# Kernel tuning notes

Measured on AMD Instinct MI355X. Metric: run time of the kernel, lower is better.

Reference implementation:

```python
import jax, jax.numpy as jnp
import numpy as np

N_EMBEDS = 1024
N_HEADS = 16
HEAD_DIM = N_EMBEDS // N_HEADS
SCALE = HEAD_DIM ** (-0.5)
B, T = 2, 2048


def setup_inputs() -> dict:
    key = jax.random.key(0)
    k1, k2, k3, k4 = jax.random.split(key, 4)
    x = jax.random.normal(k1, (B, T, N_EMBEDS), dtype=jnp.float32)
    # Glorot-uniform-style init like keras Dense defaults (scale irrelevant for correctness)
    w_qkv = jax.random.normal(k2, (N_EMBEDS, 3 * N_EMBEDS), dtype=jnp.float32) * (N_EMBEDS ** -0.5)
    w_proj = jax.random.normal(k3, (N_EMBEDS, N_EMBEDS), dtype=jnp.float32) * (N_EMBEDS ** -0.5)
    b_proj = jnp.zeros((N_EMBEDS,), dtype=jnp.float32)
    return {"x": x, "w_qkv": w_qkv, "w_proj": w_proj, "b_proj": b_proj}


def reference(x, w_qkv, w_proj, b_proj):
    Bc, Tc, D = x.shape
    qkv = x @ w_qkv                                   # [B,T,3D]
    q, k, v = jnp.split(qkv, 3, axis=-1)
    def heads(t):
        return t.reshape(Bc, Tc, N_HEADS, HEAD_DIM).transpose(0, 2, 1, 3)  # [B,H,T,hd]
    q, k, v = heads(q), heads(k), heads(v)
    att = jnp.einsum("bhqd,bhkd->bhqk", q, k) * SCALE  # [B,H,T,T]
    causal = jnp.tril(jnp.ones((Tc, Tc), dtype=bool))[None, None]
    att = jnp.where(causal, att, jnp.float32(-1e9))
    att = jax.nn.softmax(att, axis=-1)
    out = jnp.einsum("bhqk,bhkd->bhqd", att, v)        # [B,H,T,hd]
    out = out.transpose(0, 2, 1, 3).reshape(Bc, Tc, D)
    return out @ w_proj + b_proj
```

## Files before the change

### kernel.cpp

```cpp
#include <hip/hip_runtime.h>
#include <hip/hip_bf16.h>


typedef __bf16 bf16;
typedef float f32x4 __attribute__((ext_vector_type(4)));
typedef float f32x16 __attribute__((ext_vector_type(16)));
typedef bf16 bf16x4 __attribute__((ext_vector_type(4)));
typedef bf16 bf16x8 __attribute__((ext_vector_type(8)));

#define B_ 2
#define T_ 2048
#define D_ 1024
#define H_ 16
#define HD_ 64
#define QSPLIT 9

__device__ __forceinline__ f32x16 mfma32(bf16x8 a, bf16x8 b, f32x16 c) {
    return __builtin_amdgcn_mfma_f32_32x32x16_bf16(a, b, c, 0, 0, 0);
}

__device__ __forceinline__ void gload16(void* l, const void* g) {
    __builtin_amdgcn_global_load_lds(
        (const __attribute__((address_space(1))) unsigned int*)g,
        (__attribute__((address_space(3))) unsigned int*)l, 16, 0, 0);
}

__device__ __forceinline__ f32x16 z16() {
    f32x16 v;
#pragma unroll
    for (int i = 0; i < 16; ++i) v[i] = 0.f;
    return v;
}

__global__ __launch_bounds__(256) void cast_f32_bf16(const float* __restrict__ in,
                                                     bf16* __restrict__ out, int n4) {
    int i = blockIdx.x * 256 + threadIdx.x;
    if (i < n4) {
        float4 v = ((const float4*)in)[i];
        bf16x4 o = { (bf16)v.x, (bf16)v.y, (bf16)v.z, (bf16)v.w };
        ((bf16x4*)out)[i] = o;
    }
}

__global__ __launch_bounds__(256) void cast_transpose(const float* __restrict__ in,
                                                      bf16* __restrict__ out, int R, int C) {
    __shared__ float tile[32][33];
    int cx = blockIdx.x * 32 + threadIdx.x;
    int r0 = blockIdx.y * 32;
#pragma unroll
    for (int j = 0; j < 32; j += 8)
        tile[threadIdx.y + j][threadIdx.x] = in[(size_t)(r0 + threadIdx.y + j) * C + cx];
    __syncthreads();
    int rx = r0 + threadIdx.x;
    int c0 = blockIdx.x * 32;
#pragma unroll
    for (int j = 0; j < 32; j += 8)
        out[(size_t)(c0 + threadIdx.y + j) * R + rx] = (bf16)tile[threadIdx.x][threadIdx.y + j];
}

__global__ __launch_bounds__(256) void transpose_v(const bf16* __restrict__ vb,
                                                   bf16* __restrict__ vt) {
    __shared__ bf16 st[64 * 65];
    const int bh = blockIdx.y;
    const int t0 = blockIdx.x * 64;
    const int tid = threadIdx.x;
#pragma unroll
    for (int c = 0; c < 2; ++c) {
        int cid = tid + c * 256;
        int r = cid >> 3, col = (cid & 7) * 8;
        bf16x8 v = *(const bf16x8*)&vb[((size_t)bh * T_ + t0 + r) * HD_ + col];
#pragma unroll
        for (int j = 0; j < 8; ++j) st[r * 65 + col + j] = v[j];
    }
    __syncthreads();
#pragma unroll
    for (int c = 0; c < 2; ++c) {
        int cid = tid + c * 256;
        int tg = cid & 7, d = cid >> 3;
        bf16x8 o;
#pragma unroll
        for (int j = 0; j < 8; ++j) o[j] = st[(tg * 8 + j) * 65 + d];
        *(bf16x8*)&vt[((size_t)bh * HD_ + d) * T_ + t0 + tg * 8] = o;
    }
}

template <int MW, int NWN, int EPI>
__global__ __launch_bounds__(256) void gemm_k(
    const bf16* __restrict__ A, const bf16* __restrict__ Bt,
    int M, int N, int K,
    bf16* __restrict__ qb, bf16* __restrict__ kb, bf16* __restrict__ vb,
    const float* __restrict__ bias, float* __restrict__ outf) {
    constexpr int BM = 64 * MW;
    constexpr int BN = 64 * NWN;
    __shared__ bf16 sA[BM * 64];
    __shared__ bf16 sB[BN * 64];
    const int tid = threadIdx.x;
    const int wave = tid >> 6, lane = tid & 63;
    const int ln = lane & 31, hi = lane >> 5;
    const int wr = (wave >> 1) * (32 * MW);
    const int wc = (wave & 1) * (32 * NWN);
    const int m0 = blockIdx.x * BM, n0 = blockIdx.y * BN;

    f32x16 acc[MW][NWN];
#pragma unroll
    for (int mi = 0; mi < MW; ++mi)
#pragma unroll
        for (int ni = 0; ni < NWN; ++ni) acc[mi][ni] = z16();

    for (int k0 = 0; k0 < K; k0 += 64) {
        __syncthreads();
#pragma unroll
        for (int j = 0; j < 2 * MW; ++j) {
            int c = tid + 256 * j;
            int r = c >> 3, g = (c & 7) ^ (r & 7);
            gload16(&sA[c * 8], A + (size_t)(m0 + r) * K + k0 + 8 * g);
        }
#pragma unroll
        for (int j = 0; j < 2 * NWN; ++j) {
            int c = tid + 256 * j;
            int r = c >> 3, g = (c & 7) ^ (r & 7);
            gload16(&sB[c * 8], Bt + (size_t)(n0 + r) * K + k0 + 8 * g);
        }
        __syncthreads();
#pragma unroll
        for (int s = 0; s < 4; ++s) {
            bf16x8 av[MW], bv[NWN];
#pragma unroll
            for (int mi = 0; mi < MW; ++mi) {
                int r = wr + mi * 32 + ln;
                av[mi] = *(const bf16x8*)((const char*)sA + r * 128 +
                                          ((((s << 1) | hi) ^ (r & 7)) << 4));
            }
#pragma unroll
            for (int ni = 0; ni < NWN; ++ni) {
                int r = wc + ni * 32 + ln;
                bv[ni] = *(const bf16x8*)((const char*)sB + r * 128 +
                                          ((((s << 1) | hi) ^ (r & 7)) << 4));
            }
#pragma unroll
            for (int mi = 0; mi < MW; ++mi)
#pragma unroll
                for (int ni = 0; ni < NWN; ++ni)
                    acc[mi][ni] = mfma32(av[mi], bv[ni], acc[mi][ni]);
        }
    }

#pragma unroll
    for (int mi = 0; mi < MW; ++mi)
#pragma unroll
        for (int ni = 0; ni < NWN; ++ni)
#pragma unroll
            for (int r = 0; r < 16; ++r) {
                int row = m0 + wr + mi * 32 + (r & 3) + 8 * (r >> 2) + 4 * hi;
                int col = n0 + wc + ni * 32 + ln;
                float v = acc[mi][ni][r];
                if (EPI == 0) {
                    int part = col >> 10, h = (col >> 6) & 15, d = col & 63;
                    int b = row >> 11, t = row & (T_ - 1);
                    size_t idx = ((size_t)(b * H_ + h) * T_ + t) * HD_ + d;
                    bf16* dst = (part == 0) ? qb : (part == 1) ? kb : vb;
                    dst[idx] = (bf16)v;
                } else {
                    outf[(size_t)row * N + col] = v + bias[col];
                }
            }
}

__device__ __forceinline__ bf16x8 kread(const char* base, int row, int s, int hi) {
    int b = (row * 128 + s * 32 + hi * 16) ^ ((row & 7) << 4);
    return *(const bf16x8*)(base + b);
}
__device__ __forceinline__ bf16x8 vread(const char* base, int row, int s, int hi) {
    int sw = (row & 7) << 4;
    int b0 = (row * 128 + s * 32 + hi * 8) ^ sw;
    int b1 = (row * 128 + s * 32 + hi * 8 + 16) ^ sw;
    bf16x4 lo = *(const bf16x4*)(base + b0);
    bf16x4 hi4 = *(const bf16x4*)(base + b1);
    return __builtin_shufflevector(lo, hi4, 0, 1, 2, 3, 4, 5, 6, 7);
}

__global__ __launch_bounds__(256) void attn_kernel(
    const bf16* __restrict__ qb, const bf16* __restrict__ kb,
    const bf16* __restrict__ vtb, bf16* __restrict__ ob,
    bf16* __restrict__ oP, float2* __restrict__ mlP) {
    __shared__ bf16 sK2[2][4096];
    __shared__ bf16 sV2[2][4096];

    const int bid = blockIdx.x;
    const int bh = bid & 31;
    const int sid = bid >> 5;
    int qt, seg, t0, t1;
    if (sid < QSPLIT) {
        qt = sid; seg = -1; t0 = 0; t1 = 2 * qt + 2;
    } else {
        int idx = sid - QSPLIT;
        qt = QSPLIT + (idx >> 1);
        seg = idx & 1;
        if (seg == 0) { t0 = 0; t1 = qt + 1; }
        else          { t0 = qt + 1; t1 = 2 * qt + 2; }
    }
    const int b = bh >> 4, h = bh & 15;
    const int tid = threadIdx.x, wave = tid >> 6, lane = tid & 63;
    const int ln = lane & 31, hi = lane >> 5;
    const int qs = qt * 128 + wave * 32;
    const int qrow = qs + ln;

    const bf16* Qg = qb + (size_t)bh * (T_ * HD_);
    const bf16* Kg = kb + (size_t)bh * (T_ * HD_);
    const bf16* Vtg = vtb + (size_t)bh * (HD_ * T_);

    bf16x8 qf[4];
#pragma unroll
    for (int s = 0; s < 4; ++s) {
        bf16x8 v = *(const bf16x8*)&Qg[(size_t)qrow * HD_ + s * 16 + hi * 8];
#pragma unroll
        for (int e = 0; e < 8; ++e) v[e] = (bf16)((float)v[e] * 0.1803368801f);
        qf[s] = v;
    }

    const int srow = tid >> 3;
    const int scol = (tid & 7) * 8;
    const int kw0 = (srow * 128 + (tid & 7) * 16) ^ ((srow & 7) << 4);
    const int kw1 = ((srow + 32) * 128 + (tid & 7) * 16) ^ ((srow & 7) << 4);

    {
        int kv0 = t0 * 64;
        bf16x8 k0 = *(const bf16x8*)&Kg[(size_t)(kv0 + srow) * HD_ + scol];
        bf16x8 k1 = *(const bf16x8*)&Kg[(size_t)(kv0 + srow + 32) * HD_ + scol];
        bf16x8 v0 = *(const bf16x8*)&Vtg[(size_t)srow * T_ + kv0 + scol];
        bf16x8 v1 = *(const bf16x8*)&Vtg[(size_t)(srow + 32) * T_ + kv0 + scol];
        *(bf16x8*)((char*)sK2[0] + kw0) = k0;
        *(bf16x8*)((char*)sK2[0] + kw1) = k1;
        *(bf16x8*)((char*)sV2[0] + kw0) = v0;
        *(bf16x8*)((char*)sV2[0] + kw1) = v1;
    }
    __syncthreads();

    const float NINF = -__builtin_inff();
    f32x16 oA = z16(), oB = z16();
    float mR = NINF, lR = 0.f;
    int cur = 0;

    for (int t = t0; t < t1; ++t) {
        bf16x8 kr0, kr1, vr0, vr1;
        const bool pf = (t + 1) < t1;
        if (pf) {
            int kv0 = (t + 1) * 64;
            kr0 = *(const bf16x8*)&Kg[(size_t)(kv0 + srow) * HD_ + scol];
            kr1 = *(const bf16x8*)&Kg[(size_t)(kv0 + srow + 32) * HD_ + scol];
            vr0 = *(const bf16x8*)&Vtg[(size_t)srow * T_ + kv0 + scol];
            vr1 = *(const bf16x8*)&Vtg[(size_t)(srow + 32) * T_ + kv0 + scol];
        }

        if (64 * t <= qs + 31) {
            const char* kbase = (const char*)sK2[cur];
            const char* vbase = (const char*)sV2[cur];

            f32x16 p0 = z16(), p1 = z16();
#pragma unroll
            for (int s = 0; s < 4; ++s) {
                bf16x8 a0 = kread(kbase, ln, s, hi);
                bf16x8 a1 = kread(kbase, ln + 32, s, hi);
                p0 = mfma32(a0, qf[s], p0);
                p1 = mfma32(a1, qf[s], p1);
            }

            if (64 * t + 63 > qs) {
                int kvb = 64 * t + 4 * hi;
#pragma unroll
                for (int r = 0; r < 16; ++r) {
                    int kvr = kvb + (r & 3) + 8 * (r >> 2);
                    if (kvr > qrow) p0[r] = NINF;
                    if (kvr + 32 > qrow) p1[r] = NINF;
                }
            }

            float mx0 = NINF, mx1 = NINF, mx2 = NINF, mx3 = NINF;
#pragma unroll
            for (int r = 0; r < 16; r += 4) {
                mx0 = fmaxf(mx0, p0[r]);     mx1 = fmaxf(mx1, p0[r + 1]);
                mx2 = fmaxf(mx2, p0[r + 2]); mx3 = fmaxf(mx3, p0[r + 3]);
                mx0 = fmaxf(mx0, p1[r]);     mx1 = fmaxf(mx1, p1[r + 1]);
                mx2 = fmaxf(mx2, p1[r + 2]); mx3 = fmaxf(mx3, p1[r + 3]);
            }
            float pm = fmaxf(fmaxf(mx0, mx1), fmaxf(mx2, mx3));
            pm = fmaxf(pm, __shfl_xor(pm, 32));

            if (__any(pm > mR + 8.f)) {
                float mnew = fmaxf(mR, pm);
                float fac = exp2f(mR - mnew);
                lR *= fac;
#pragma unroll
                for (int r = 0; r < 16; ++r) { oA[r] *= fac; oB[r] *= fac; }
                mR = mnew;
            }

            float s0 = 0.f, s1 = 0.f, s2 = 0.f, s3 = 0.f;
#pragma unroll
            for (int r = 0; r < 16; r += 4) {
                p0[r] = exp2f(p0[r] - mR);         s0 += p0[r];
                p0[r + 1] = exp2f(p0[r + 1] - mR); s1 += p0[r + 1];
                p0[r + 2] = exp2f(p0[r + 2] - mR); s2 += p0[r + 2];
                p0[r + 3] = exp2f(p0[r + 3] - mR); s3 += p0[r + 3];
                p1[r] = exp2f(p1[r] - mR);         s0 += p1[r];
                p1[r + 1] = exp2f(p1[r + 1] - mR); s1 += p1[r + 1];
                p1[r + 2] = exp2f(p1[r + 2] - mR); s2 += p1[r + 2];
                p1[r + 3] = exp2f(p1[r + 3] - mR); s3 += p1[r + 3];
            }
            float rs = (s0 + s1) + (s2 + s3);
            rs += __shfl_xor(rs, 32);
            lR += rs;

            bf16x8 pa0, pa1, pa2, pa3;
#pragma unroll
            for (int e = 0; e < 8; ++e) {
                pa0[e] = (bf16)p0[e];
                pa1[e] = (bf16)p0[8 + e];
                pa2[e] = (bf16)p1[e];
                pa3[e] = (bf16)p1[8 + e];
            }

#pragma unroll
            for (int s = 0; s < 4; ++s) {
                bf16x8 pas = (s == 0) ? pa0 : (s == 1) ? pa1 : (s == 2) ? pa2 : pa3;
                oA = mfma32(vread(vbase, ln, s, hi), pas, oA);
                oB = mfma32(vread(vbase, ln + 32, s, hi), pas, oB);
            }
        }

        if (pf) {
            int nb = cur ^ 1;
            *(bf16x8*)((char*)sK2[nb] + kw0) = kr0;
            *(bf16x8*)((char*)sK2[nb] + kw1) = kr1;
            *(bf16x8*)((char*)sV2[nb] + kw0) = vr0;
            *(bf16x8*)((char*)sV2[nb] + kw1) = vr1;
        }
        __syncthreads();
        cur ^= 1;
    }

    if (seg < 0) {
        float inv = 1.f / lR;
        bf16* orow = ob + ((size_t)(b * T_ + qrow)) * D_ + h * HD_;
#pragma unroll
        for (int g = 0; g < 4; ++g) {
            bf16x4 w, w2;
#pragma unroll
            for (int j = 0; j < 4; ++j) {
                w[j] = (bf16)(oA[4 * g + j] * inv);
                w2[j] = (bf16)(oB[4 * g + j] * inv);
            }
            *(bf16x4*)&orow[4 * hi + 8 * g] = w;
            *(bf16x4*)&orow[32 + 4 * hi + 8 * g] = w2;
        }
    } else {
        int row = wave * 32 + ln;
        size_t sbase = (((size_t)bh * (16 - QSPLIT) + (qt - QSPLIT)) * 2 + seg);
        bf16* prow = oP + (sbase * 128 + row) * 64;
#pragma unroll
        for (int g = 0; g < 4; ++g) {
            bf16x4 w, w2;
#pragma unroll
            for (int j = 0; j < 4; ++j) {
                w[j] = (bf16)oA[4 * g + j];
                w2[j] = (bf16)oB[4 * g + j];
            }
            *(bf16x4*)&prow[4 * hi + 8 * g] = w;
            *(bf16x4*)&prow[32 + 4 * hi + 8 * g] = w2;
        }
        if (hi == 0) mlP[sbase * 128 + row] = make_float2(mR, lR);
    }
}

__global__ __launch_bounds__(256) void attn_merge(
    const bf16* __restrict__ oP, const float2* __restrict__ mlP,
    bf16* __restrict__ ob) {
    constexpr int NQS = 16 - QSPLIT;
    int gid = blockIdx.x * 256 + threadIdx.x;
    int bh = gid / (NQS * 128);
    int rem = gid - bh * (NQS * 128);
    int qi = rem >> 7, row = rem & 127;
    int b = bh >> 4, h = bh & 15;
    int t = (QSPLIT + qi) * 128 + row;
    size_t sbase = ((size_t)bh * NQS + qi) * 2;
    float2 ml0 = mlP[(sbase + 0) * 128 + row];
    float2 ml1 = mlP[(sbase + 1) * 128 + row];
    float ms = fmaxf(ml0.x, ml1.x);
    float w0 = exp2f(ml0.x - ms), w1 = exp2f(ml1.x - ms);
    float inv = 1.f / (ml0.y * w0 + ml1.y * w1);
    w0 *= inv; w1 *= inv;
    const bf16* r0 = oP + ((sbase + 0) * 128 + row) * 64;
    const bf16* r1 = oP + ((sbase + 1) * 128 + row) * 64;
    bf16* dst = ob + ((size_t)(b * T_ + t)) * D_ + h * HD_;
#pragma unroll
    for (int g = 0; g < 8; ++g) {
        bf16x8 a = *(const bf16x8*)&r0[g * 8];
        bf16x8 c = *(const bf16x8*)&r1[g * 8];
        bf16x8 o;
#pragma unroll
        for (int j = 0; j < 8; ++j)
            o[j] = (bf16)((float)a[j] * w0 + (float)c[j] * w1);
        *(bf16x8*)&dst[g * 8] = o;
    }
}

extern "C" void kernel_launch(void* const* d_in, const int* in_sizes, int n_in,
                              void* d_out, int out_size, void* d_ws, size_t ws_size,
                              hipStream_t stream) {
    const float* x = (const float*)d_in[0];
    const float* w_qkv = (const float*)d_in[1];
    const float* w_proj = (const float*)d_in[2];
    const float* b_proj = (const float*)d_in[3];
    float* out = (float*)d_out;
    char* ws = (char*)d_ws;

    bf16* xb = (bf16*)(ws);
    bf16* ob = (bf16*)(ws);
    bf16* wqkvt = (bf16*)(ws + 8388608);
    bf16* vtbuf = (bf16*)(ws + 8388608);
    bf16* qbuf = (bf16*)(ws + 16777216);
    bf16* wprojt = (bf16*)(ws + 16777216);
    bf16* kbuf = (bf16*)(ws + 25165824);
    bf16* vbuf = (bf16*)(ws + 33554432);
    bf16* oP = (bf16*)(ws + 33554432);
    float2* mlP = (float2*)(ws + 33554432 + 7340032);

    cast_f32_bf16<<<4096, 256, 0, stream>>>(x, xb, (B_ * T_ * D_) / 4);
    dim3 tb(32, 8);
    cast_transpose<<<dim3(3 * D_ / 32, D_ / 32), tb, 0, stream>>>(w_qkv, wqkvt, D_, 3 * D_);

    gemm_k<2, 2, 0><<<dim3((B_ * T_) / 128, (3 * D_) / 128), 256, 0, stream>>>(
        xb, wqkvt, B_ * T_, 3 * D_, D_, qbuf, kbuf, vbuf, nullptr, nullptr);

    transpose_v<<<dim3(T_ / 64, B_ * H_), 256, 0, stream>>>(vbuf, vtbuf);

    attn_kernel<<<23 * 32, 256, 0, stream>>>(qbuf, kbuf, vtbuf, ob, oP, mlP);
    attn_merge<<<112, 256, 0, stream>>>(oP, mlP, ob);

    cast_transpose<<<dim3(D_ / 32, D_ / 32), tb, 0, stream>>>(w_proj, wprojt, D_, D_);

    gemm_k<1, 2, 1><<<dim3((B_ * T_) / 64, D_ / 128), 256, 0, stream>>>(
        ob, wprojt, B_ * T_, D_, D_, nullptr, nullptr, nullptr, b_proj, out);
}
```

Baseline: 135.7 us.

## Stream K/V tiles into LDS via direct global_load_lds with swizzled source addresses

Replaces the register-staged K/V prefetch (global load to VGPRs, then ds_write after compute) with direct global-to-LDS loads into the alternate buffer. The XOR swizzle moves from the LDS write address to the global source column. It also adds s_setprio around the MFMA blocks, fuses exp2 with the bf16 packing of P, and requests 3 blocks per CU through launch_bounds. The aim is to cut VGPR pressure and LDS-write instructions and raise occupancy, at the cost of register spilling if the cap at 3 waves is too tight.

```diff
diff --git a/kernel.cpp b/kernel.cpp
--- a/kernel.cpp
+++ b/kernel.cpp
@@ -179,7 +179,7 @@
     return __builtin_shufflevector(lo, hi4, 0, 1, 2, 3, 4, 5, 6, 7);
 }
 
-__global__ __launch_bounds__(256) void attn_kernel(
+__global__ __launch_bounds__(256, 3) void attn_kernel(
     const bf16* __restrict__ qb, const bf16* __restrict__ kb,
     const bf16* __restrict__ vtb, bf16* __restrict__ ob,
     bf16* __restrict__ oP, float2* __restrict__ mlP) {
@@ -218,21 +218,15 @@
         qf[s] = v;
     }
 
-    const int srow = tid >> 3;
-    const int scol = (tid & 7) * 8;
-    const int kw0 = (srow * 128 + (tid & 7) * 16) ^ ((srow & 7) << 4);
-    const int kw1 = ((srow + 32) * 128 + (tid & 7) * 16) ^ ((srow & 7) << 4);
+    const int rr0 = tid >> 3;
+    const int gg = ((tid & 7) ^ (rr0 & 7)) * 8;
 
     {
         int kv0 = t0 * 64;
-        bf16x8 k0 = *(const bf16x8*)&Kg[(size_t)(kv0 + srow) * HD_ + scol];
-        bf16x8 k1 = *(const bf16x8*)&Kg[(size_t)(kv0 + srow + 32) * HD_ + scol];
-        bf16x8 v0 = *(const bf16x8*)&Vtg[(size_t)srow * T_ + kv0 + scol];
-        bf16x8 v1 = *(const bf16x8*)&Vtg[(size_t)(srow + 32) * T_ + kv0 + scol];
-        *(bf16x8*)((char*)sK2[0] + kw0) = k0;
-        *(bf16x8*)((char*)sK2[0] + kw1) = k1;
-        *(bf16x8*)((char*)sV2[0] + kw0) = v0;
-        *(bf16x8*)((char*)sV2[0] + kw1) = v1;
+        gload16(&sK2[0][tid * 8], Kg + (size_t)(kv0 + rr0) * HD_ + gg);
+        gload16(&sK2[0][(tid + 256) * 8], Kg + (size_t)(kv0 + rr0 + 32) * HD_ + gg);
+        gload16(&sV2[0][tid * 8], Vtg + (size_t)rr0 * T_ + kv0 + gg);
+        gload16(&sV2[0][(tid + 256) * 8], Vtg + (size_t)(rr0 + 32) * T_ + kv0 + gg);
     }
     __syncthreads();
 
@@ -242,14 +236,14 @@
     int cur = 0;
 
     for (int t = t0; t < t1; ++t) {
-        bf16x8 kr0, kr1, vr0, vr1;
-        const bool pf = (t + 1) < t1;
-        if (pf) {
+        if ((t + 1) < t1) {
             int kv0 = (t + 1) * 64;
-            kr0 = *(const bf16x8*)&Kg[(size_t)(kv0 + srow) * HD_ + scol];
-            kr1 = *(const bf16x8*)&Kg[(size_t)(kv0 + srow + 32) * HD_ + scol];
-            vr0 = *(const bf16x8*)&Vtg[(size_t)srow * T_ + kv0 + scol];
-            vr1 = *(const bf16x8*)&Vtg[(size_t)(srow + 32) * T_ + kv0 + scol];
+            bf16* kd = sK2[cur ^ 1];
+            bf16* vd = sV2[cur ^ 1];
+            gload16(&kd[tid * 8], Kg + (size_t)(kv0 + rr0) * HD_ + gg);
+            gload16(&kd[(tid + 256) * 8], Kg + (size_t)(kv0 + rr0 + 32) * HD_ + gg);
+            gload16(&vd[tid * 8], Vtg + (size_t)rr0 * T_ + kv0 + gg);
+            gload16(&vd[(tid + 256) * 8], Vtg + (size_t)(rr0 + 32) * T_ + kv0 + gg);
         }
 
         if (64 * t <= qs + 31) {
@@ -257,6 +251,7 @@
             const char* vbase = (const char*)sV2[cur];
 
             f32x16 p0 = z16(), p1 = z16();
+            __builtin_amdgcn_s_setprio(1);
 #pragma unroll
             for (int s = 0; s < 4; ++s) {
                 bf16x8 a0 = kread(kbase, ln, s, hi);
@@ -264,6 +259,7 @@
                 p0 = mfma32(a0, qf[s], p0);
                 p1 = mfma32(a1, qf[s], p1);
             }
+            __builtin_amdgcn_s_setprio(0);
 
             if (64 * t + 63 > qs) {
                 int kvb = 64 * t + 4 * hi;
@@ -296,45 +292,28 @@
             }
 
             float s0 = 0.f, s1 = 0.f, s2 = 0.f, s3 = 0.f;
-#pragma unroll
-            for (int r = 0; r < 16; r += 4) {
-                p0[r] = exp2f(p0[r] - mR);         s0 += p0[r];
-                p0[r + 1] = exp2f(p0[r + 1] - mR); s1 += p0[r + 1];
-                p0[r + 2] = exp2f(p0[r + 2] - mR); s2 += p0[r + 2];
-                p0[r + 3] = exp2f(p0[r + 3] - mR); s3 += p0[r + 3];
-                p1[r] = exp2f(p1[r] - mR);         s0 += p1[r];
-                p1[r + 1] = exp2f(p1[r + 1] - mR); s1 += p1[r + 1];
-                p1[r + 2] = exp2f(p1[r + 2] - mR); s2 += p1[r + 2];
-                p1[r + 3] = exp2f(p1[r + 3] - mR); s3 += p1[r + 3];
+            bf16x8 pa0, pa1, pa2, pa3;
+#pragma unroll
+            for (int e = 0; e < 8; ++e) {
+                float a = exp2f(p0[e] - mR);      s0 += a;  pa0[e] = (bf16)a;
+                float bb = exp2f(p0[8 + e] - mR); s1 += bb; pa1[e] = (bf16)bb;
+                float c = exp2f(p1[e] - mR);      s2 += c;  pa2[e] = (bf16)c;
+                float d = exp2f(p1[8 + e] - mR);  s3 += d;  pa3[e] = (bf16)d;
             }
             float rs = (s0 + s1) + (s2 + s3);
             rs += __shfl_xor(rs, 32);
             lR += rs;
 
-            bf16x8 pa0, pa1, pa2, pa3;
-#pragma unroll
-            for (int e = 0; e < 8; ++e) {
-                pa0[e] = (bf16)p0[e];
-                pa1[e] = (bf16)p0[8 + e];
-                pa2[e] = (bf16)p1[e];
-                pa3[e] = (bf16)p1[8 + e];
-            }
-
+            __builtin_amdgcn_s_setprio(1);
 #pragma unroll
             for (int s = 0; s < 4; ++s) {
                 bf16x8 pas = (s == 0) ? pa0 : (s == 1) ? pa1 : (s == 2) ? pa2 : pa3;
                 oA = mfma32(vread(vbase, ln, s, hi), pas, oA);
                 oB = mfma32(vread(vbase, ln + 32, s, hi), pas, oB);
             }
-        }
-
-        if (pf) {
-            int nb = cur ^ 1;
-            *(bf16x8*)((char*)sK2[nb] + kw0) = kr0;
-            *(bf16x8*)((char*)sK2[nb] + kw1) = kr1;
-            *(bf16x8*)((char*)sV2[nb] + kw0) = vr0;
-            *(bf16x8*)((char*)sV2[nb] + kw1) = vr1;
-        }
+            __builtin_amdgcn_s_setprio(0);
+        }
+
         __syncthreads();
         cur ^= 1;
     }
```

Result: faster. 124.8 us (-8.0%).
